# Performance work log

Hardware: AMD Instinct MI355X
Metric: run time of the kernel (lower is better)

Reference implementation:

```python
import jax, jax.numpy as jnp
import numpy as np

EMBED_DIM = 1024
NUM_HEADS = 16
HEAD_DIM = EMBED_DIM // NUM_HEADS
SCALING = (1.0 / HEAD_DIM) ** 0.5


def setup_inputs() -> dict:
    key = jax.random.key(0)
    ks = jax.random.split(key, 9)
    d = EMBED_DIM
    return {
        "hidden_states": jax.random.normal(ks[0], (4, 2048, d), dtype=jnp.float32),
        "q_w": jax.random.normal(ks[1], (d, d), dtype=jnp.float32) * 0.02,
        "q_b": jax.random.normal(ks[2], (d,), dtype=jnp.float32) * 0.02,
        "k_w": jax.random.normal(ks[3], (d, d), dtype=jnp.float32) * 0.02,
        "k_b": jax.random.normal(ks[4], (d,), dtype=jnp.float32) * 0.02,
        "v_w": jax.random.normal(ks[5], (d, d), dtype=jnp.float32) * 0.02,
        "v_b": jax.random.normal(ks[6], (d,), dtype=jnp.float32) * 0.02,
        "out_w": jax.random.normal(ks[7], (d, d), dtype=jnp.float32) * 0.02,
        "out_b": jax.random.normal(ks[8], (d,), dtype=jnp.float32) * 0.02,
    }


def _shape(x, bsz, seq, nh, hd):
    # [B, T, E] -> [B, H, T, Hd]
    return x.reshape(bsz, seq, nh, hd).transpose(0, 2, 1, 3)


def reference(hidden_states, q_w, q_b, k_w, k_b, v_w, v_b, out_w, out_b):
    bsz, tgt_len, _ = hidden_states.shape
    # torch Linear: y = x @ W.T + b; query scaled by sqrt(1/head_dim)
    q = (hidden_states @ q_w.T + q_b) * SCALING
    k = hidden_states @ k_w.T + k_b
    v = hidden_states @ v_w.T + v_b
    q = _shape(q, bsz, tgt_len, NUM_HEADS, HEAD_DIM)
    k = _shape(k, bsz, tgt_len, NUM_HEADS, HEAD_DIM)
    v = _shape(v, bsz, tgt_len, NUM_HEADS, HEAD_DIM)
    # [B, H, T, S]
    attn_weights = jnp.einsum("bhtd,bhsd->bhts", q, k)
    attn_weights = jax.nn.softmax(attn_weights, axis=-1)
    # [B, H, T, Hd] -> [B, T, E]
    attn_output = jnp.einsum("bhts,bhsd->bhtd", attn_weights, v)
    attn_output = attn_output.transpose(0, 2, 1, 3).reshape(bsz, tgt_len, EMBED_DIM)
    return attn_output @ out_w.T + out_b
```

## Files before the change

kernel.cpp:

```cpp
#include <hip/hip_runtime.h>
#include <hip/hip_bf16.h>
#include <cstdint>
#include <math.h>

typedef uint16_t u16;
typedef __attribute__((ext_vector_type(8))) short short8;
typedef __attribute__((ext_vector_type(4))) float floatx4;
typedef __attribute__((ext_vector_type(16))) float floatx16;

__device__ __forceinline__ float bf2f(u16 u) {
  return __uint_as_float(((uint32_t)u) << 16);
}
__device__ __forceinline__ u16 f2bf(float f) {
  uint32_t u = __float_as_uint(f);
  u += 0x7FFF + ((u >> 16) & 1);
  return (u16)(u >> 16);
}

__device__ __forceinline__ void glds16(const void* g, void* l) {
  __builtin_amdgcn_global_load_lds(
      (const __attribute__((address_space(1))) void*)g,
      (__attribute__((address_space(3))) void*)l, 16, 0, 0);
}

__device__ __forceinline__ bool detect_fp32(const u16* __restrict__ hs) {
  int big = 0;
#pragma unroll
  for (int i = 0; i < 128; ++i) {
    const int e = (hs[i] >> 7) & 0xFF;
    big += (e >= 140);
  }
  return big > 0;
}

__device__ __forceinline__ void conv_blk(
    const void* __restrict__ src, u16* __restrict__ dst, int i, bool f32)
{
  if (f32) {
    const float4 v = ((const float4*)src)[i];
    ushort4 d;
    d.x = f2bf(v.x); d.y = f2bf(v.y); d.z = f2bf(v.z); d.w = f2bf(v.w);
    ((ushort4*)dst)[i] = d;
  } else {
    ((ushort4*)dst)[i] = ((const ushort4*)src)[i];
  }
}

__global__ __launch_bounds__(256) void convert_all(
    const void* __restrict__ hs, const void* __restrict__ qw,
    const void* __restrict__ kw, const void* __restrict__ vw,
    const void* __restrict__ ow, const void* __restrict__ qb,
    const void* __restrict__ kb, const void* __restrict__ vb,
    const void* __restrict__ ob,
    u16* __restrict__ d_hs, u16* __restrict__ d_qw, u16* __restrict__ d_kw,
    u16* __restrict__ d_vw, u16* __restrict__ d_ow, u16* __restrict__ d_qb,
    u16* __restrict__ d_kb, u16* __restrict__ d_vb, u16* __restrict__ d_ob)
{
  const bool f32 = detect_fp32((const u16*)hs);
  const int bid = blockIdx.x;
  const int tid = threadIdx.x;
  if (bid < 8192) {
    conv_blk(hs, d_hs, bid * 256 + tid, f32);
  } else if (bid < 8192 + 4096) {
    const int w = (bid - 8192) >> 10;
    const int i = ((bid - 8192) & 1023) * 256 + tid;
    const void* s = (w == 0) ? qw : (w == 1) ? kw : (w == 2) ? vw : ow;
    u16* d        = (w == 0) ? d_qw : (w == 1) ? d_kw : (w == 2) ? d_vw : d_ow;
    conv_blk(s, d, i, f32);
  } else {
    const int w = bid - 12288;
    const void* s = (w == 0) ? qb : (w == 1) ? kb : (w == 2) ? vb : ob;
    u16* d        = (w == 0) ? d_qb : (w == 1) ? d_kb : (w == 2) ? d_vb : d_ob;
    conv_blk(s, d, tid, f32);
  }
}

template <int MODE>
__device__ __forceinline__ void gemm_body(
    const u16* __restrict__ A, const u16* __restrict__ W,
    const u16* __restrict__ bias, void* __restrict__ vout,
    float scale, u16* As, u16* Bs, int bx, int by, bool f32out)
{
  constexpr int KD = 1024;
  const int tid  = threadIdx.x;
  const int lane = tid & 63;
  const int l15  = lane & 15;
  const int quad = lane >> 4;
  const int wid  = tid >> 6;
  const int bm = by * 128, bn = bx * 128;
  const int wm = (wid >> 1) * 64, wn = (wid & 1) * 64;

  floatx4 acc[4][4];
#pragma unroll
  for (int i = 0; i < 4; ++i)
#pragma unroll
    for (int j = 0; j < 4; ++j)
#pragma unroll
      for (int r = 0; r < 4; ++r) acc[i][j][r] = 0.0f;

  const int c0 = tid, c1 = tid + 256;
  const u16* Ag0 = A + (size_t)(bm + (c0 >> 2)) * KD + (c0 & 3) * 8;
  const u16* Ag1 = A + (size_t)(bm + (c1 >> 2)) * KD + (c1 & 3) * 8;
  const u16* Wg0 = W + (size_t)(bn + (c0 >> 2)) * KD + (c0 & 3) * 8;
  const u16* Wg1 = W + (size_t)(bn + (c1 >> 2)) * KD + (c1 & 3) * 8;
  u16* As0 = As + c0 * 8;  u16* As1 = As + c1 * 8;
  u16* Bs0 = Bs + c0 * 8;  u16* Bs1 = Bs + c1 * 8;

  for (int kt = 0; kt < KD / 32; ++kt) {
    const int ko = kt * 32;
    glds16(Ag0 + ko, As0);
    glds16(Ag1 + ko, As1);
    glds16(Wg0 + ko, Bs0);
    glds16(Wg1 + ko, Bs1);
    __syncthreads();
    short8 af[4], bf[4];
#pragma unroll
    for (int mb = 0; mb < 4; ++mb)
      af[mb] = *(const short8*)&As[(wm + mb * 16 + l15) * 32 + quad * 8];
#pragma unroll
    for (int nb = 0; nb < 4; ++nb)
      bf[nb] = *(const short8*)&Bs[(wn + nb * 16 + l15) * 32 + quad * 8];
#pragma unroll
    for (int mb = 0; mb < 4; ++mb)
#pragma unroll
      for (int nb = 0; nb < 4; ++nb) {
        if (MODE == 2)
          acc[mb][nb] = __builtin_amdgcn_mfma_f32_16x16x32_bf16(
              bf[nb], af[mb], acc[mb][nb], 0, 0, 0);
        else
          acc[mb][nb] = __builtin_amdgcn_mfma_f32_16x16x32_bf16(
              af[mb], bf[nb], acc[mb][nb], 0, 0, 0);
      }
    __syncthreads();
  }

  if (MODE == 2) {
#pragma unroll
    for (int nb = 0; nb < 4; ++nb)
#pragma unroll
      for (int r = 0; r < 4; ++r) {
        const int wrow = bn + wn + nb * 16 + quad * 4 + r;
        const float bv = bf2f(bias[wrow]);
        const int h = wrow >> 6, d = wrow & 63;
        u16* out = (u16*)vout;
#pragma unroll
        for (int mb = 0; mb < 4; ++mb) {
          const int tcol = bm + wm + mb * 16 + l15;
          const int b = tcol >> 11, t = tcol & 2047;
          out[((size_t)(b * 16 + h) * 64 + d) * 2048 + t] =
              f2bf((acc[mb][nb][r] + bv) * scale);
        }
      }
  } else {
    float bias_v[4];
#pragma unroll
    for (int nb = 0; nb < 4; ++nb) bias_v[nb] = bf2f(bias[bn + wn + nb * 16 + l15]);
#pragma unroll
    for (int mb = 0; mb < 4; ++mb)
#pragma unroll
      for (int nb = 0; nb < 4; ++nb)
#pragma unroll
        for (int r = 0; r < 4; ++r) {
          const int row = bm + wm + mb * 16 + quad * 4 + r;
          const int col = bn + wn + nb * 16 + l15;
          const float v = (acc[mb][nb][r] + bias_v[nb]) * scale;
          if (MODE == 0) {
            if (f32out) ((float*)vout)[(size_t)row * 1024 + col] = v;
            else        ((u16*)vout)[(size_t)row * 1024 + col] = f2bf(v);
          } else {
            const int b = row >> 11, t = row & 2047;
            const int h = col >> 6, d = col & 63;
            ((u16*)vout)[(((size_t)(b * 16 + h)) * 2048 + t) * 64 + d] = f2bf(v);
          }
        }
  }
}

__global__ __launch_bounds__(256, 3) void gemm_qkv(
    const u16* __restrict__ A,
    const u16* __restrict__ Wq, const u16* __restrict__ Wk, const u16* __restrict__ Wv,
    const u16* __restrict__ bq, const u16* __restrict__ bk, const u16* __restrict__ bv,
    u16* __restrict__ Oq, u16* __restrict__ Ok, u16* __restrict__ Ov)
{
  __shared__ u16 As[128 * 32];
  __shared__ u16 Bs[128 * 32];
  const int z = blockIdx.z;
  if (z < 2) {
    const u16* W    = z ? Wk : Wq;
    const u16* bias = z ? bk : bq;
    u16* out        = z ? Ok : Oq;
    const float scale = z ? 1.0f : 0.125f;
    gemm_body<1>(A, W, bias, out, scale, As, Bs, blockIdx.x, blockIdx.y, false);
  } else {
    gemm_body<2>(A, Wv, bv, Ov, 1.0f, As, Bs, blockIdx.x, blockIdx.y, false);
  }
}

__global__ __launch_bounds__(256, 3) void gemm_out_proj(
    const u16* __restrict__ A, const u16* __restrict__ W,
    const u16* __restrict__ bias, void* __restrict__ out,
    const u16* __restrict__ probe)
{
  __shared__ u16 As[128 * 32];
  __shared__ u16 Bs[128 * 32];
  const bool f32 = detect_fp32(probe);
  gemm_body<0>(A, W, bias, out, 1.0f, As, Bs, blockIdx.x, blockIdx.y, f32);
}

__global__ __launch_bounds__(256, 4) void attn_fused(
    const u16* __restrict__ Q, const u16* __restrict__ K,
    const u16* __restrict__ VT, u16* __restrict__ O)
{
  constexpr int T = 2048, D = 64;
  constexpr int KS = 72;
  constexpr int VS = 136;
  __shared__ u16 Ks[128 * KS];
  __shared__ u16 Vts[64 * VS];
  __shared__ float Linv[128];

  const int tid  = threadIdx.x;
  const int lane = tid & 63;
  const int l31  = lane & 31;
  const int half = lane >> 5;
  const int wid  = tid >> 6;
  const int bh = blockIdx.y;
  const int qt = blockIdx.x;
  const int q0w = wid * 32;

  const u16* Qb = Q + (size_t)bh * T * D + (size_t)qt * 128 * D;
  const u16* Kb = K + (size_t)bh * T * D;
  const u16* Vb = VT + (size_t)bh * D * T;

  short8 qf[4];
#pragma unroll
  for (int kk = 0; kk < 4; ++kk)
    qf[kk] = *(const short8*)&Qb[(q0w + l31) * D + kk * 16 + half * 8];

  floatx16 o_acc[2];
#pragma unroll
  for (int dt = 0; dt < 2; ++dt)
#pragma unroll
    for (int i = 0; i < 16; ++i) o_acc[dt][i] = 0.0f;
  float lA = 0.0f, lB = 0.0f;

#pragma unroll 1
  for (int kt = 0; kt < T / 128; ++kt) {
    const u16* Kt = Kb + (size_t)kt * 128 * D;
#pragma unroll
    for (int j = 0; j < 4; ++j) {
      const int c = tid + j * 256;
      const int r = c >> 3, d0 = (c & 7) * 8;
      *(short8*)&Ks[r * KS + d0] = *(const short8*)&Kt[r * D + d0];
    }
#pragma unroll
    for (int j = 0; j < 4; ++j) {
      const int c = tid + j * 256;
      const int d = c >> 4, toff = (c & 15) * 8;
      *(short8*)&Vts[d * VS + toff] =
          *(const short8*)&Vb[(size_t)d * T + kt * 128 + toff];
    }
    __syncthreads();

#pragma unroll
    for (int t = 0; t < 4; ++t) {
      floatx16 s;
#pragma unroll
      for (int i = 0; i < 16; ++i) s[i] = 0.0f;
#pragma unroll
      for (int kk = 0; kk < 4; ++kk) {
        const short8 kf = *(const short8*)&Ks[(t * 32 + l31) * KS + kk * 16 + half * 8];
        s = __builtin_amdgcn_mfma_f32_32x32x16_bf16(kf, qf[kk], s, 0, 0, 0);
      }
      uint32_t e[4][2];
#pragma unroll
      for (int g = 0; g < 4; ++g) {
        const float p0 = __expf(fminf((float)s[4 * g + 0], 30.f));
        const float p1 = __expf(fminf((float)s[4 * g + 1], 30.f));
        const float p2 = __expf(fminf((float)s[4 * g + 2], 30.f));
        const float p3 = __expf(fminf((float)s[4 * g + 3], 30.f));
        lA += p0 + p1;
        lB += p2 + p3;
        const uint32_t u0 = __float_as_uint(p0) + 0x8000u;
        const uint32_t u1 = __float_as_uint(p1) + 0x8000u;
        const uint32_t u2 = __float_as_uint(p2) + 0x8000u;
        const uint32_t u3 = __float_as_uint(p3) + 0x8000u;
        e[g][0] = __builtin_amdgcn_perm(u1, u0, 0x07060302);
        e[g][1] = __builtin_amdgcn_perm(u3, u2, 0x07060302);
      }
#pragma unroll
      for (int c = 0; c < 2; ++c) {
        const uint32_t x0 = half ? e[2 * c][0] : e[2 * c + 1][0];
        const uint32_t x1 = half ? e[2 * c][1] : e[2 * c + 1][1];
        const uint32_t r0 = (uint32_t)__shfl_xor((int)x0, 32);
        const uint32_t r1 = (uint32_t)__shfl_xor((int)x1, 32);
        union { uint32_t u[4]; short8 v; } pu;
        pu.u[0] = half ? r0 : e[2 * c][0];
        pu.u[1] = half ? r1 : e[2 * c][1];
        pu.u[2] = half ? e[2 * c + 1][0] : r0;
        pu.u[3] = half ? e[2 * c + 1][1] : r1;
        const short8 pf = pu.v;
        const int kkp = 2 * t + c;
        const short8 vf0 = *(const short8*)&Vts[l31 * VS + kkp * 16 + half * 8];
        const short8 vf1 = *(const short8*)&Vts[(32 + l31) * VS + kkp * 16 + half * 8];
        o_acc[0] = __builtin_amdgcn_mfma_f32_32x32x16_bf16(pf, vf0, o_acc[0], 0, 0, 0);
        o_acc[1] = __builtin_amdgcn_mfma_f32_32x32x16_bf16(pf, vf1, o_acc[1], 0, 0, 0);
      }
    }
    __syncthreads();
  }

  const float l_acc = lA + lB;
  const float l_full = l_acc + __shfl_xor(l_acc, 32);
  Linv[q0w + l31] = 1.0f / l_full;

  const int b = bh >> 4, h = bh & 15;
  u16* Ob = O + ((size_t)b * 2048 + (size_t)qt * 128) * 1024 + h * 64;
  float invs[16];
#pragma unroll
  for (int i = 0; i < 16; ++i)
    invs[i] = Linv[q0w + (i & 3) + 8 * (i >> 2) + 4 * half];
#pragma unroll
  for (int dt = 0; dt < 2; ++dt)
#pragma unroll
    for (int i = 0; i < 16; ++i) {
      const int qrow = q0w + (i & 3) + 8 * (i >> 2) + 4 * half;
      Ob[(size_t)qrow * 1024 + dt * 32 + l31] = f2bf((float)o_acc[dt][i] * invs[i]);
    }
}

extern "C" void kernel_launch(void* const* d_in, const int* in_sizes, int n_in,
                              void* d_out, int out_size, void* d_ws, size_t ws_size,
                              hipStream_t stream) {
  const u16* hs_probe = (const u16*)d_in[0];

  const size_t TE = (size_t)4 * 2048 * 1024;
  const size_t WE = (size_t)1024 * 1024;
  u16* hsB = (u16*)d_ws;
  u16* Qb  = hsB + TE;
  u16* Kb  = Qb + TE;
  u16* Vb  = Kb + TE;
  u16* Ob  = Vb + TE;
  u16* qwB = Ob + TE;
  u16* kwB = qwB + WE;
  u16* vwB = kwB + WE;
  u16* owB = vwB + WE;
  u16* qbB = owB + WE;
  u16* kbB = qbB + 1024;
  u16* vbB = kbB + 1024;
  u16* obB = vbB + 1024;

  dim3 bb(256);
  convert_all<<<dim3(12292), bb, 0, stream>>>(
      d_in[0], d_in[1], d_in[3], d_in[5], d_in[7],
      d_in[2], d_in[4], d_in[6], d_in[8],
      hsB, qwB, kwB, vwB, owB, qbB, kbB, vbB, obB);

  gemm_qkv<<<dim3(8, 64, 3), bb, 0, stream>>>(
      hsB, qwB, kwB, vwB, qbB, kbB, vbB, Qb, Kb, Vb);
  attn_fused<<<dim3(16, 64), bb, 0, stream>>>(Qb, Kb, Vb, Ob);
  gemm_out_proj<<<dim3(8, 64), bb, 0, stream>>>(Ob, owB, obB, d_out, hs_probe);
}
```

Measured before the change: 344.2 us.

## Prefetch next K/V tile into registers and streamline softmax in attention kernel

The attention kernel now loads the next K/V tile into registers while the current tile is computed, which removes one of the two barriers per iteration and hides global load latency. The softmax switches to native exp2 by folding log2(e) into the Q scale, packs to bf16 with a hardware pack-convert instruction, and exchanges wave halves with permlane32 swaps instead of shuffles. MFMA sections are wrapped in setprio raises. The register prefetch increases VGPR pressure, which may reduce occupancy, and the pack-convert rounding differs slightly from the old manual rounding.

Result: slower. 453.4 us (+31.7%).

```diff
diff --git a/kernel.cpp b/kernel.cpp
--- a/kernel.cpp
+++ b/kernel.cpp
@@ -16,6 +16,12 @@
   u += 0x7FFF + ((u >> 16) & 1);
   return (u16)(u >> 16);
 }
+
+#if __has_builtin(__builtin_amdgcn_exp2f)
+#define EXP2(x) __builtin_amdgcn_exp2f(x)
+#else
+#define EXP2(x) __expf((x) * 0.6931471805599453f)
+#endif
 
 __device__ __forceinline__ void glds16(const void* g, void* l) {
   __builtin_amdgcn_global_load_lds(
@@ -189,7 +195,7 @@
     const u16* W    = z ? Wk : Wq;
     const u16* bias = z ? bk : bq;
     u16* out        = z ? Ok : Oq;
-    const float scale = z ? 1.0f : 0.125f;
+    const float scale = z ? 1.0f : 0.18033688f;
     gemm_body<1>(A, W, bias, out, scale, As, Bs, blockIdx.x, blockIdx.y, false);
   } else {
     gemm_body<2>(A, Wv, bv, Ov, 1.0f, As, Bs, blockIdx.x, blockIdx.y, false);
@@ -212,6 +218,7 @@
     const u16* __restrict__ VT, u16* __restrict__ O)
 {
   constexpr int T = 2048, D = 64;
+  constexpr int NT = T / 128;
   constexpr int KS = 72;
   constexpr int VS = 136;
   __shared__ u16 Ks[128 * KS];
@@ -243,74 +250,83 @@
     for (int i = 0; i < 16; ++i) o_acc[dt][i] = 0.0f;
   float lA = 0.0f, lB = 0.0f;
 
+  short8 krg[4], vrg[4];
+#pragma unroll
+  for (int j = 0; j < 4; ++j) {
+    const int c = tid + j * 256;
+    krg[j] = *(const short8*)&Kb[(size_t)(c >> 3) * D + (c & 7) * 8];
+    vrg[j] = *(const short8*)&Vb[(size_t)(c >> 4) * T + (c & 15) * 8];
+  }
+
 #pragma unroll 1
-  for (int kt = 0; kt < T / 128; ++kt) {
-    const u16* Kt = Kb + (size_t)kt * 128 * D;
+  for (int kt = 0; kt < NT; ++kt) {
+    if (kt) __syncthreads();
 #pragma unroll
     for (int j = 0; j < 4; ++j) {
       const int c = tid + j * 256;
-      const int r = c >> 3, d0 = (c & 7) * 8;
-      *(short8*)&Ks[r * KS + d0] = *(const short8*)&Kt[r * D + d0];
-    }
-#pragma unroll
-    for (int j = 0; j < 4; ++j) {
-      const int c = tid + j * 256;
-      const int d = c >> 4, toff = (c & 15) * 8;
-      *(short8*)&Vts[d * VS + toff] =
-          *(const short8*)&Vb[(size_t)d * T + kt * 128 + toff];
+      *(short8*)&Ks[(c >> 3) * KS + (c & 7) * 8] = krg[j];
+      *(short8*)&Vts[(c >> 4) * VS + (c & 15) * 8] = vrg[j];
     }
     __syncthreads();
+    if (kt + 1 < NT) {
+      const u16* Kt = Kb + (size_t)(kt + 1) * 128 * D;
+      const u16* Vt = Vb + (size_t)(kt + 1) * 128;
+#pragma unroll
+      for (int j = 0; j < 4; ++j) {
+        const int c = tid + j * 256;
+        krg[j] = *(const short8*)&Kt[(size_t)(c >> 3) * D + (c & 7) * 8];
+        vrg[j] = *(const short8*)&Vt[(size_t)(c >> 4) * T + (c & 15) * 8];
+      }
+    }
 
 #pragma unroll
     for (int t = 0; t < 4; ++t) {
       floatx16 s;
 #pragma unroll
       for (int i = 0; i < 16; ++i) s[i] = 0.0f;
+      __builtin_amdgcn_s_setprio(1);
 #pragma unroll
       for (int kk = 0; kk < 4; ++kk) {
         const short8 kf = *(const short8*)&Ks[(t * 32 + l31) * KS + kk * 16 + half * 8];
         s = __builtin_amdgcn_mfma_f32_32x32x16_bf16(kf, qf[kk], s, 0, 0, 0);
       }
+      __builtin_amdgcn_s_setprio(0);
       uint32_t e[4][2];
 #pragma unroll
       for (int g = 0; g < 4; ++g) {
-        const float p0 = __expf(fminf((float)s[4 * g + 0], 30.f));
-        const float p1 = __expf(fminf((float)s[4 * g + 1], 30.f));
-        const float p2 = __expf(fminf((float)s[4 * g + 2], 30.f));
-        const float p3 = __expf(fminf((float)s[4 * g + 3], 30.f));
+        const float p0 = EXP2(fminf((float)s[4 * g + 0], 44.f));
+        const float p1 = EXP2(fminf((float)s[4 * g + 1], 44.f));
+        const float p2 = EXP2(fminf((float)s[4 * g + 2], 44.f));
+        const float p3 = EXP2(fminf((float)s[4 * g + 3], 44.f));
         lA += p0 + p1;
         lB += p2 + p3;
-        const uint32_t u0 = __float_as_uint(p0) + 0x8000u;
-        const uint32_t u1 = __float_as_uint(p1) + 0x8000u;
-        const uint32_t u2 = __float_as_uint(p2) + 0x8000u;
-        const uint32_t u3 = __float_as_uint(p3) + 0x8000u;
-        e[g][0] = __builtin_amdgcn_perm(u1, u0, 0x07060302);
-        e[g][1] = __builtin_amdgcn_perm(u3, u2, 0x07060302);
+        asm("v_cvt_pk_bf16_f32 %0, %1, %2" : "=v"(e[g][0]) : "v"(p0), "v"(p1));
+        asm("v_cvt_pk_bf16_f32 %0, %1, %2" : "=v"(e[g][1]) : "v"(p2), "v"(p3));
       }
 #pragma unroll
       for (int c = 0; c < 2; ++c) {
-        const uint32_t x0 = half ? e[2 * c][0] : e[2 * c + 1][0];
-        const uint32_t x1 = half ? e[2 * c][1] : e[2 * c + 1][1];
-        const uint32_t r0 = (uint32_t)__shfl_xor((int)x0, 32);
-        const uint32_t r1 = (uint32_t)__shfl_xor((int)x1, 32);
+        uint32_t a0 = e[2 * c][0], b0 = e[2 * c + 1][0];
+        uint32_t a1 = e[2 * c][1], b1 = e[2 * c + 1][1];
+        asm("v_permlane32_swap_b32 %0, %1" : "+v"(a0), "+v"(b0));
+        asm("v_permlane32_swap_b32 %0, %1" : "+v"(a1), "+v"(b1));
         union { uint32_t u[4]; short8 v; } pu;
-        pu.u[0] = half ? r0 : e[2 * c][0];
-        pu.u[1] = half ? r1 : e[2 * c][1];
-        pu.u[2] = half ? e[2 * c + 1][0] : r0;
-        pu.u[3] = half ? e[2 * c + 1][1] : r1;
+        pu.u[0] = a0; pu.u[1] = a1; pu.u[2] = b0; pu.u[3] = b1;
         const short8 pf = pu.v;
         const int kkp = 2 * t + c;
         const short8 vf0 = *(const short8*)&Vts[l31 * VS + kkp * 16 + half * 8];
         const short8 vf1 = *(const short8*)&Vts[(32 + l31) * VS + kkp * 16 + half * 8];
+        __builtin_amdgcn_s_setprio(1);
         o_acc[0] = __builtin_amdgcn_mfma_f32_32x32x16_bf16(pf, vf0, o_acc[0], 0, 0, 0);
         o_acc[1] = __builtin_amdgcn_mfma_f32_32x32x16_bf16(pf, vf1, o_acc[1], 0, 0, 0);
+        __builtin_amdgcn_s_setprio(0);
       }
     }
-    __syncthreads();
   }
 
   const float l_acc = lA + lB;
-  const float l_full = l_acc + __shfl_xor(l_acc, 32);
+  uint32_t lu0 = __float_as_uint(l_acc), lu1 = lu0;
+  asm("v_permlane32_swap_b32 %0, %1" : "+v"(lu0), "+v"(lu1));
+  const float l_full = l_acc + __uint_as_float(half ? lu0 : lu1);
   Linv[q0w + l31] = 1.0f / l_full;
 
   const int b = bh >> 4, h = bh & 15;
```
